# Kernel optimization log

Measured on AMD Instinct MI355X. Metric: run time of the kernel, lower is better.

The kernel has to match this reference:

```python
import jax, jax.numpy as jnp
import numpy as np
from jax import lax

B, C, H, W, HEADS = 2, 256, 192, 256, 8
HS = C // 2  # hidden_size per axial branch


def setup_inputs() -> dict:
    key = jax.random.key(0)
    ks = jax.random.split(key, 12)
    f = lambda k, shape, s=0.02: jax.random.normal(k, shape, jnp.float32) * s
    return {
        "x": jax.random.normal(ks[0], (B, C, H, W), jnp.float32),
        "ln1_g": jnp.ones((C,), jnp.float32),
        "ln1_b": jnp.zeros((C,), jnp.float32),
        "conv_in_w": f(ks[1], (C, C)),
        "conv_in_b": jnp.zeros((C,), jnp.float32),
        "qkv_h_w": f(ks[2], (3 * HS, HS)),
        "qkv_h_b": jnp.zeros((3 * HS,), jnp.float32),
        "qkv_v_w": f(ks[3], (3 * HS, HS)),
        "qkv_v_b": jnp.zeros((3 * HS,), jnp.float32),
        "fuse_w": f(ks[4], (C, C)),
        "fuse_b": jnp.zeros((C,), jnp.float32),
        "ln2_g": jnp.ones((C,), jnp.float32),
        "ln2_b": jnp.zeros((C,), jnp.float32),
        "fc1_w": f(ks[5], (4 * C, C)),
        "fc1_b": f(ks[6], (4 * C,), 1e-6),
        "fc2_w": f(ks[7], (C, 4 * C)),
        "fc2_b": f(ks[8], (C,), 1e-6),
        "peg_w": f(ks[9], (C, 1, 3, 3)),
        "peg_b": jnp.zeros((C,), jnp.float32),
    }


def _ln(x, g, b, eps=1e-5):
    m = x.mean(-1, keepdims=True)
    v = jnp.mean((x - m) ** 2, axis=-1, keepdims=True)
    return (x - m) / jnp.sqrt(v + eps) * g + b


def _mha(q, k, v, heads):
    # q,k,v: [Bn, N, Ch]
    Bn, N, Ch = q.shape
    d = Ch // heads
    q = q.reshape(Bn, N, heads, d).transpose(0, 2, 1, 3)
    k = k.reshape(Bn, N, heads, d).transpose(0, 2, 1, 3)
    v = v.reshape(Bn, N, heads, d).transpose(0, 2, 1, 3)
    scores = jnp.einsum('bhnd,bhmd->bhnm', q, k) / jnp.sqrt(jnp.float32(d))
    probs = jax.nn.softmax(scores, axis=-1)
    out = jnp.einsum('bhnm,bhmd->bhnd', probs, v)
    return out.transpose(0, 2, 1, 3).reshape(Bn, N, Ch)


def reference(x, ln1_g, ln1_b, conv_in_w, conv_in_b, qkv_h_w, qkv_h_b,
              qkv_v_w, qkv_v_b, fuse_w, fuse_b, ln2_g, ln2_b,
              fc1_w, fc1_b, fc2_w, fc2_b, peg_w, peg_b):
    Bx, Cx, Hx, Wx = x.shape
    hs = Cx // 2
    h0 = x
    # LayerNorm over channel dim
    t = x.reshape(Bx, Cx, Hx * Wx).transpose(0, 2, 1)  # [B, HW, C]
    t = _ln(t, ln1_g, ln1_b)
    xn = t.transpose(0, 2, 1).reshape(Bx, Cx, Hx, Wx)
    # 1x1 conv input
    ci = jnp.einsum('bchw,oc->bohw', xn, conv_in_w) + conv_in_b[None, :, None, None]
    # horizontal strips: [B*H, W, hs]; vertical strips: [B*W, H, hs]
    fh = ci[:, :hs].transpose(0, 2, 3, 1).reshape(Bx * Hx, Wx, hs)
    fv = ci[:, hs:].transpose(0, 3, 2, 1).reshape(Bx * Wx, Hx, hs)
    q_h, k_h, v_h = jnp.split(fh @ qkv_h_w.T + qkv_h_b, 3, axis=2)
    q_v, k_v, v_v = jnp.split(fv @ qkv_v_w.T + qkv_v_b, 3, axis=2)
    ah = _mha(q_h, k_h, v_h, HEADS)  # [B*H, W, hs]
    av = _mha(q_v, k_v, v_v, HEADS)  # [B*W, H, hs]
    ah = ah.reshape(Bx, Hx, Wx, hs).transpose(0, 3, 1, 2)  # [B, hs, H, W]
    av = av.reshape(Bx, Wx, Hx, hs).transpose(0, 3, 2, 1)  # [B, hs, H, W]
    cat = jnp.concatenate((ah, av), axis=1)  # [B, C, H, W]
    attn_out = jnp.einsum('bchw,oc->bohw', cat, fuse_w) + fuse_b[None, :, None, None]
    x1 = attn_out + h0
    # FFN
    t = x1.reshape(Bx, Cx, Hx * Wx).transpose(0, 2, 1)  # [B, HW, C]
    h1 = t
    t2 = _ln(t, ln2_g, ln2_b)
    t2 = jax.nn.gelu(t2 @ fc1_w.T + fc1_b, approximate=False)
    t2 = t2 @ fc2_w.T + fc2_b
    t = t2 + h1
    x2 = t.transpose(0, 2, 1).reshape(Bx, Cx, Hx, Wx)
    # PEG: depthwise 3x3 conv + residual
    peg = lax.conv_general_dilated(
        x2, peg_w, window_strides=(1, 1), padding='SAME',
        dimension_numbers=('NCHW', 'OIHW', 'NCHW'), feature_group_count=Cx)
    return peg + peg_b[None, :, None, None] + x2
```

## Files before the change

kernel.cpp:

```cpp
#include <hip/hip_runtime.h>

#define B_ 2
#define C_ 256
#define H_ 192
#define W_ 256
#define HW_ 49152
#define T_ 98304

typedef __bf16 bf16x8 __attribute__((ext_vector_type(8)));
typedef float  f32x4  __attribute__((ext_vector_type(4)));
typedef short  s16x8  __attribute__((ext_vector_type(8)));

__device__ inline unsigned short f2bf(float f) {
    unsigned u = __float_as_uint(f);
    u = u + 0x7fffu + ((u >> 16) & 1u);
    return (unsigned short)(u >> 16);
}
__device__ inline float bf2f(unsigned short u) {
    return __uint_as_float(((unsigned)u) << 16);
}
__device__ inline unsigned short bfbits(float f) {
    __bf16 h = (__bf16)f;
    return __builtin_bit_cast(unsigned short, h);
}

__global__ __launch_bounds__(256) void wcvt_kernel(
    const float* __restrict__ in, unsigned short* __restrict__ out, int n)
{
    int i = (blockIdx.x * 256 + threadIdx.x) * 4;
    if (i >= n) return;
    float4 v = *(const float4*)(in + i);
    out[i + 0] = f2bf(v.x);
    out[i + 1] = f2bf(v.y);
    out[i + 2] = f2bf(v.z);
    out[i + 3] = f2bf(v.w);
}

__global__ __launch_bounds__(256) void ln1_stats_kernel(
    const float* __restrict__ x, float* __restrict__ mean, float* __restrict__ rstd)
{
    int t = blockIdx.x * 256 + threadIdx.x;
    int b = t / HW_;
    int hw = t - b * HW_;
    const float* p = x + (size_t)b * C_ * HW_ + hw;
    float s = 0.f, q = 0.f;
    for (int c = 0; c < C_; ++c) {
        float v = p[(size_t)c * HW_];
        s += v; q += v * v;
    }
    float m = s * (1.f / C_);
    float var = q * (1.f / C_) - m * m;
    mean[t] = m;
    rstd[t] = rsqrtf(var + 1e-5f);
}

__global__ __launch_bounds__(256) void ln2_stats_kernel(
    const float* __restrict__ xr, float* __restrict__ mean, float* __restrict__ rstd)
{
    int wv = threadIdx.x >> 6, lane = threadIdx.x & 63;
    int t = blockIdx.x * 4 + wv;
    const float4 v = *(const float4*)(xr + (size_t)t * C_ + lane * 4);
    float s = v.x + v.y + v.z + v.w;
    float q = v.x * v.x + v.y * v.y + v.z * v.z + v.w * v.w;
    #pragma unroll
    for (int o = 32; o > 0; o >>= 1) {
        s += __shfl_xor(s, o);
        q += __shfl_xor(q, o);
    }
    if (lane == 0) {
        float m = s * (1.f / C_);
        float var = q * (1.f / C_) - m * m;
        mean[t] = m;
        rstd[t] = rsqrtf(var + 1e-5f);
    }
}

__global__ __launch_bounds__(256) void xln_kernel(
    const float* __restrict__ x, const float* __restrict__ mean,
    const float* __restrict__ rstd, const float* __restrict__ g,
    const float* __restrict__ bta, unsigned short* __restrict__ xn)
{
    __shared__ float tile[32][33];
    int t0 = blockIdx.x * 32;
    int c0 = blockIdx.y * 32;
    int b = t0 / HW_, hw0 = t0 - b * HW_;
    int tid = threadIdx.x, lane = tid & 31, grp = tid >> 5;
    float mm = mean[t0 + lane], rr = rstd[t0 + lane];
    #pragma unroll
    for (int j = 0; j < 4; ++j) {
        int c = grp + j * 8;
        float v = x[((size_t)b * C_ + c0 + c) * HW_ + hw0 + lane];
        tile[c][lane] = (v - mm) * rr;
    }
    __syncthreads();
    float gg = g[c0 + lane], bb = bta[c0 + lane];
    #pragma unroll
    for (int j = 0; j < 4; ++j) {
        int tt = grp + j * 8;
        xn[(size_t)(t0 + tt) * C_ + c0 + lane] = f2bf(tile[lane][tt] * gg + bb);
    }
}

enum { AB_ROW = 0, AB_CAT = 1, AB_GATHER = 2, AF32_LN = 3 };
enum { EB_BF16 = 0, EB_F32 = 1, EG_BF16 = 2, ER_F32 = 3 };

template<int AMODE, int EMODE>
__global__ __launch_bounds__(256) void mgemm(
    const unsigned short* __restrict__ A0, const unsigned short* __restrict__ A1,
    const float* __restrict__ Af,
    const unsigned short* __restrict__ Wb, const float* __restrict__ bias,
    const float* __restrict__ mean, const float* __restrict__ rstd,
    const float* __restrict__ lng, const float* __restrict__ lnb,
    const float* __restrict__ resid, float* __restrict__ outf,
    unsigned short* __restrict__ outb,
    int K, int lda, int ldw, int ldo, int rowoff)
{
    __shared__ __align__(16) short As[8][512];
    __shared__ __align__(16) short Bs[8][512];
    const int tid = threadIdx.x;
    const int t0 = blockIdx.x * 128;
    const int n0 = blockIdx.y * 128;
    const int lane = tid & 63, wv = tid >> 6;
    const int wr = wv >> 1, wc = wv & 1;

    f32x4 acc[4][4];
    #pragma unroll
    for (int m = 0; m < 4; ++m)
        #pragma unroll
        for (int n = 0; n < 4; ++n)
            acc[m][n] = (f32x4){0.f, 0.f, 0.f, 0.f};

    for (int k0 = 0; k0 < K; k0 += 32) {
        #pragma unroll
        for (int ic = 0; ic < 2; ++ic) {
            const int c = ic * 256 + tid;
            const int r = c >> 2;
            const int kk = (c & 3) * 8;
            const int slot = (((r & 15) | ((kk >> 3) << 4))) * 8;
            s16x8 v;
            if (AMODE == AF32_LN) {
                const float* src = Af + (size_t)(t0 + r) * lda + k0 + kk;
                float4 v0 = *(const float4*)src;
                float4 v1 = *(const float4*)(src + 4);
                const float mm = mean[t0 + r], rr = rstd[t0 + r];
                float4 g0 = *(const float4*)(lng + k0 + kk);
                float4 g1 = *(const float4*)(lng + k0 + kk + 4);
                float4 b0 = *(const float4*)(lnb + k0 + kk);
                float4 b1 = *(const float4*)(lnb + k0 + kk + 4);
                v[0] = (short)f2bf((v0.x - mm) * rr * g0.x + b0.x);
                v[1] = (short)f2bf((v0.y - mm) * rr * g0.y + b0.y);
                v[2] = (short)f2bf((v0.z - mm) * rr * g0.z + b0.z);
                v[3] = (short)f2bf((v0.w - mm) * rr * g0.w + b0.w);
                v[4] = (short)f2bf((v1.x - mm) * rr * g1.x + b1.x);
                v[5] = (short)f2bf((v1.y - mm) * rr * g1.y + b1.y);
                v[6] = (short)f2bf((v1.z - mm) * rr * g1.z + b1.z);
                v[7] = (short)f2bf((v1.w - mm) * rr * g1.w + b1.w);
            } else {
                const unsigned short* src;
                if (AMODE == AB_CAT) {
                    src = (k0 < 128)
                        ? A0 + (size_t)(t0 + r) * 128 + k0 + kk
                        : A1 + (size_t)(t0 + r) * 128 + (k0 - 128) + kk;
                } else if (AMODE == AB_GATHER) {
                    const int gr = rowoff + t0 + r;
                    const int b = gr / HW_;
                    const int rem = gr - b * HW_;
                    const int w = rem / H_;
                    const int h = rem - w * H_;
                    src = A0 + ((size_t)b * HW_ + (size_t)h * W_ + w) * 256
                          + 128 + k0 + kk;
                } else {
                    src = A0 + (size_t)(t0 + r) * lda + k0 + kk;
                }
                v = *(const s16x8*)src;
            }
            *(s16x8*)&As[r >> 4][slot] = v;
            s16x8 wv8 = *(const s16x8*)(Wb + (size_t)(n0 + r) * ldw + k0 + kk);
            *(s16x8*)&Bs[r >> 4][slot] = wv8;
        }
        __syncthreads();
        bf16x8 af[4], bfr[4];
        #pragma unroll
        for (int m = 0; m < 4; ++m)
            af[m] = __builtin_bit_cast(bf16x8, *(const s16x8*)&As[wr * 4 + m][lane * 8]);
        #pragma unroll
        for (int n = 0; n < 4; ++n)
            bfr[n] = __builtin_bit_cast(bf16x8, *(const s16x8*)&Bs[wc * 4 + n][lane * 8]);
        #pragma unroll
        for (int m = 0; m < 4; ++m)
            #pragma unroll
            for (int n = 0; n < 4; ++n)
                acc[m][n] = __builtin_amdgcn_mfma_f32_16x16x32_bf16(
                    af[m], bfr[n], acc[m][n], 0, 0, 0);
        __syncthreads();
    }

    const int rowb = t0 + wr * 64 + (lane >> 4) * 4;
    const int colb = n0 + wc * 64 + (lane & 15);
    #pragma unroll
    for (int n = 0; n < 4; ++n) {
        const int col = colb + n * 16;
        const float bcol = bias[col];
        #pragma unroll
        for (int m = 0; m < 4; ++m) {
            #pragma unroll
            for (int r = 0; r < 4; ++r) {
                const int row = rowb + m * 16 + r;
                float v = acc[m][n][r] + bcol;
                if (EMODE == EG_BF16)
                    v = 0.5f * v * (1.f + erff(v * 0.70710678118654752f));
                if (EMODE == ER_F32)
                    v += resid[(size_t)row * 256 + col];
                if (EMODE == EB_F32 || EMODE == ER_F32)
                    outf[(size_t)row * ldo + col] = v;
                else
                    outb[(size_t)row * ldo + col] = f2bf(v);
            }
        }
    }
}

__global__ __launch_bounds__(256) void tadd_kernel(
    const float* __restrict__ x, float* __restrict__ x1)
{
    __shared__ float tile[32][33];
    int t0 = blockIdx.x * 32;
    int c0 = blockIdx.y * 32;
    int b = t0 / HW_, hw0 = t0 - b * HW_;
    int tid = threadIdx.x;
    int lane = tid & 31, grp = tid >> 5;
    #pragma unroll
    for (int j = 0; j < 4; ++j) {
        int c = grp + j * 8;
        tile[c][lane] = x[((size_t)b * C_ + c0 + c) * HW_ + hw0 + lane];
    }
    __syncthreads();
    #pragma unroll
    for (int j = 0; j < 4; ++j) {
        int tt = grp + j * 8;
        x1[(size_t)(t0 + tt) * C_ + c0 + lane] += tile[lane][tt];
    }
}

template<int N, int DIR>
__global__ __launch_bounds__(256) void attn_mfma_kernel(
    const unsigned short* __restrict__ qkv, unsigned short* __restrict__ outb, int strip0)
{
    constexpr int NT = N / 16;
    constexpr int CH = N / 32;
    constexpr int QTW = N / 64;
    constexpr int PST = N + 8;
    __shared__ __align__(16) short kls[NT * 256];
    __shared__ __align__(16) short vls[CH * 512];
    __shared__ __align__(16) short plds[4 * 16 * PST];
    const int head = blockIdx.x & 7;
    const int sl = blockIdx.x >> 3;
    const int s = strip0 + sl;
    const int tid = threadIdx.x;
    const unsigned short* base = qkv + (size_t)sl * N * 384;
    for (int i = tid; i < 2 * N; i += 256) {
        int r = i >> 1, hf = i & 1;
        s16x8 kv = *(const s16x8*)(base + (size_t)r * 384 + 128 + head * 16 + hf * 8);
        *(s16x8*)&kls[(r >> 4) * 256 + (hf * 16 + (r & 15)) * 8] = kv;
    }
    for (int i = tid; i < 2 * N; i += 256) {
        int r = i >> 1, hf = i & 1;
        s16x8 vv = *(const s16x8*)(base + (size_t)r * 384 + 256 + head * 16 + hf * 8);
        short* dst = &vls[(r >> 5) * 512 + ((r & 31) >> 3) * 128 + (r & 7)];
        #pragma unroll
        for (int j = 0; j < 8; ++j)
            dst[(hf * 8 + j) * 8] = vv[j];
    }
    __syncthreads();
    const int wv = tid >> 6, lane = tid & 63, g = lane >> 4, q = lane & 15;
    short* myP = &plds[wv * 16 * PST];
    const bf16x8 zf = __builtin_bit_cast(bf16x8, (s16x8){0,0,0,0,0,0,0,0});
    for (int qt_i = 0; qt_i < QTW; ++qt_i) {
        const int q0 = wv * (N / 4) + qt_i * 16;
        bf16x8 qf = zf;
        if (lane < 32)
            qf = __builtin_bit_cast(bf16x8,
                *(const s16x8*)(base + (size_t)(q0 + q) * 384 + head * 16 + g * 8));
        f32x4 sc[NT];
        #pragma unroll
        for (int n = 0; n < NT; ++n) {
            bf16x8 kf = zf;
            if (lane < 32)
                kf = __builtin_bit_cast(bf16x8, *(const s16x8*)&kls[n * 256 + lane * 8]);
            sc[n] = __builtin_amdgcn_mfma_f32_16x16x32_bf16(
                kf, qf, (f32x4){0.f, 0.f, 0.f, 0.f}, 0, 0, 0);
        }
        float mx = -3.0e38f;
        #pragma unroll
        for (int n = 0; n < NT; ++n)
            mx = fmaxf(mx, fmaxf(fmaxf(sc[n][0], sc[n][1]), fmaxf(sc[n][2], sc[n][3])));
        mx = fmaxf(mx, __shfl_xor(mx, 16));
        mx = fmaxf(mx, __shfl_xor(mx, 32));
        float sum = 0.f;
        #pragma unroll
        for (int n = 0; n < NT; ++n) {
            float p0 = __expf((sc[n][0] - mx) * 0.25f);
            float p1 = __expf((sc[n][1] - mx) * 0.25f);
            float p2 = __expf((sc[n][2] - mx) * 0.25f);
            float p3 = __expf((sc[n][3] - mx) * 0.25f);
            sum += (p0 + p1) + (p2 + p3);
            unsigned u01 = ((unsigned)bfbits(p1) << 16) | bfbits(p0);
            unsigned u23 = ((unsigned)bfbits(p3) << 16) | bfbits(p2);
            *(unsigned*)&myP[q * PST + n * 16 + g * 4] = u01;
            *(unsigned*)&myP[q * PST + n * 16 + g * 4 + 2] = u23;
        }
        sum += __shfl_xor(sum, 16);
        sum += __shfl_xor(sum, 32);
        const float inv = 1.f / sum;
        f32x4 o = (f32x4){0.f, 0.f, 0.f, 0.f};
        #pragma unroll
        for (int c = 0; c < CH; ++c) {
            bf16x8 vf = __builtin_bit_cast(bf16x8, *(const s16x8*)&vls[c * 512 + lane * 8]);
            bf16x8 pf = __builtin_bit_cast(bf16x8, *(const s16x8*)&myP[q * PST + c * 32 + g * 8]);
            o = __builtin_amdgcn_mfma_f32_16x16x32_bf16(vf, pf, o, 0, 0, 0);
        }
        unsigned lo = ((unsigned)bfbits(o[1] * inv) << 16) | bfbits(o[0] * inv);
        unsigned hi = ((unsigned)bfbits(o[3] * inv) << 16) | bfbits(o[2] * inv);
        size_t dst;
        if (DIR == 0) {
            dst = ((size_t)s * W_ + q0 + q) * 128 + head * 16 + g * 4;
        } else {
            int b = s >> 8, w = s & 255;
            dst = ((size_t)b * HW_ + (size_t)(q0 + q) * W_ + w) * 128 + head * 16 + g * 4;
        }
        *(uint2*)&outb[dst] = make_uint2(lo, hi);
    }
}

__global__ __launch_bounds__(256) void peg_kernel(
    const float* __restrict__ x2t, const float* __restrict__ pw,
    const float* __restrict__ pb, float* __restrict__ outp)
{
    __shared__ float pwt[9][132];
    __shared__ float tile[128][36];
    const int t0 = blockIdx.x * 32;
    const int cbase = blockIdx.y * 128;
    const int b = t0 / HW_, hw0 = t0 - b * HW_;
    const int h = hw0 >> 8, w0 = hw0 & 255;
    const int tid = threadIdx.x;
    for (int i = tid; i < 1152; i += 256) {
        int tap = i >> 7, ch = i & 127;
        pwt[tap][ch] = pw[(size_t)(cbase + ch) * 9 + tap];
    }
    __syncthreads();
    const int c4 = tid & 31;
    const int tg = tid >> 5;
    const int cq = cbase + c4 * 4;
    float4 pb4 = *(const float4*)(pb + cq);
    #pragma unroll
    for (int j = 0; j < 4; ++j) {
        int tt = tg * 4 + j;
        int t = t0 + tt;
        int w = w0 + tt;
        float4 a = *(const float4*)(x2t + (size_t)t * C_ + cq);
        a.x += pb4.x; a.y += pb4.y; a.z += pb4.z; a.w += pb4.w;
        #pragma unroll
        for (int dh = -1; dh <= 1; ++dh) {
            int hh = h + dh;
            if (hh < 0 || hh >= H_) continue;
            #pragma unroll
            for (int dw = -1; dw <= 1; ++dw) {
                int ww = w + dw;
                if (ww < 0 || ww >= W_) continue;
                float4 xv = *(const float4*)(x2t + (size_t)(t + dh * W_ + dw) * C_ + cq);
                float4 wv = *(const float4*)&pwt[(dh + 1) * 3 + (dw + 1)][c4 * 4];
                a.x += wv.x * xv.x; a.y += wv.y * xv.y;
                a.z += wv.z * xv.z; a.w += wv.w * xv.w;
            }
        }
        tile[c4 * 4 + 0][tt] = a.x;
        tile[c4 * 4 + 1][tt] = a.y;
        tile[c4 * 4 + 2][tt] = a.z;
        tile[c4 * 4 + 3][tt] = a.w;
    }
    __syncthreads();
    const int ch = tid >> 1, hf = (tid & 1) * 16;
    float* drow = outp + ((size_t)b * C_ + cbase + ch) * HW_ + hw0 + hf;
    #pragma unroll
    for (int qq = 0; qq < 4; ++qq) {
        float4 vv = make_float4(tile[ch][hf + qq * 4 + 0], tile[ch][hf + qq * 4 + 1],
                                tile[ch][hf + qq * 4 + 2], tile[ch][hf + qq * 4 + 3]);
        *(float4*)(drow + qq * 4) = vv;
    }
}

extern "C" void kernel_launch(void* const* d_in, const int* in_sizes, int n_in,
                              void* d_out, int out_size, void* d_ws, size_t ws_size,
                              hipStream_t stream)
{
    (void)in_sizes; (void)n_in; (void)out_size; (void)ws_size;
    const float* x         = (const float*)d_in[0];
    const float* ln1_g     = (const float*)d_in[1];
    const float* ln1_b     = (const float*)d_in[2];
    const float* conv_in_w = (const float*)d_in[3];
    const float* conv_in_b = (const float*)d_in[4];
    const float* qkv_h_w   = (const float*)d_in[5];
    const float* qkv_h_b   = (const float*)d_in[6];
    const float* qkv_v_w   = (const float*)d_in[7];
    const float* qkv_v_b   = (const float*)d_in[8];
    const float* fuse_w    = (const float*)d_in[9];
    const float* fuse_b    = (const float*)d_in[10];
    const float* ln2_g     = (const float*)d_in[11];
    const float* ln2_b     = (const float*)d_in[12];
    const float* fc1_w     = (const float*)d_in[13];
    const float* fc1_b     = (const float*)d_in[14];
    const float* fc2_w     = (const float*)d_in[15];
    const float* fc2_b     = (const float*)d_in[16];
    const float* peg_w     = (const float*)d_in[17];
    const float* peg_b     = (const float*)d_in[18];
    float* outp = (float*)d_out;

    float* wsf   = (float*)d_ws;
    float* mean1 = wsf;
    float* rstd1 = wsf + (size_t)T_;
    float* mean2 = wsf + 2 * (size_t)T_;
    float* rstd2 = wsf + 3 * (size_t)T_;
    float* x1    = wsf + 4 * (size_t)T_;
    unsigned short* xn = (unsigned short*)x1;
    unsigned short* ci = (unsigned short*)(x1 + (size_t)T_ * 128);
    unsigned short* ah = (unsigned short*)(x1 + (size_t)T_ * 256);
    unsigned short* av = ah + (size_t)T_ * 128;
    unsigned short* qt = av + (size_t)T_ * 128;
    unsigned short* wb = qt + (size_t)12288 * 1024;
    unsigned short* wconv = wb;
    unsigned short* wqh   = wconv + 65536;
    unsigned short* wqv   = wqh + 49152;
    unsigned short* wfu   = wqv + 49152;
    unsigned short* wf1   = wfu + 65536;
    unsigned short* wf2   = wf1 + 262144;

    dim3 blk(256);

    wcvt_kernel<<<dim3(64), blk, 0, stream>>>(conv_in_w, wconv, 65536);
    wcvt_kernel<<<dim3(48), blk, 0, stream>>>(qkv_h_w, wqh, 49152);
    wcvt_kernel<<<dim3(48), blk, 0, stream>>>(qkv_v_w, wqv, 49152);
    wcvt_kernel<<<dim3(64), blk, 0, stream>>>(fuse_w, wfu, 65536);
    wcvt_kernel<<<dim3(256), blk, 0, stream>>>(fc1_w, wf1, 262144);
    wcvt_kernel<<<dim3(256), blk, 0, stream>>>(fc2_w, wf2, 262144);
    ln1_stats_kernel<<<dim3(T_ / 256), blk, 0, stream>>>(x, mean1, rstd1);
    xln_kernel<<<dim3(T_ / 32, 8), blk, 0, stream>>>(x, mean1, rstd1, ln1_g, ln1_b, xn);
    mgemm<AB_ROW, EB_BF16><<<dim3(768, 2), blk, 0, stream>>>(
        xn, nullptr, nullptr, wconv, conv_in_b, nullptr, nullptr, nullptr, nullptr,
        nullptr, nullptr, ci, 256, 256, 256, 256, 0);
    for (int ch = 0; ch < 4; ++ch) {
        const size_t r0 = (size_t)ch * 24576;
        mgemm<AB_ROW, EB_BF16><<<dim3(192, 3), blk, 0, stream>>>(
            ci + r0 * 256, nullptr, nullptr, wqh, qkv_h_b, nullptr, nullptr, nullptr,
            nullptr, nullptr, nullptr, qt, 128, 256, 128, 384, 0);
        attn_mfma_kernel<256, 0><<<dim3(96 * 8), blk, 0, stream>>>(qt, ah, ch * 96);
    }
    for (int cv = 0; cv < 4; ++cv) {
        mgemm<AB_GATHER, EB_BF16><<<dim3(192, 3), blk, 0, stream>>>(
            ci, nullptr, nullptr, wqv, qkv_v_b, nullptr, nullptr, nullptr,
            nullptr, nullptr, nullptr, qt, 128, 0, 128, 384, cv * 24576);
        attn_mfma_kernel<192, 1><<<dim3(128 * 8), blk, 0, stream>>>(qt, av, cv * 128);
    }
    mgemm<AB_CAT, EB_F32><<<dim3(768, 2), blk, 0, stream>>>(
        ah, av, nullptr, wfu, fuse_b, nullptr, nullptr, nullptr, nullptr,
        nullptr, x1, nullptr, 256, 128, 256, 256, 0);
    tadd_kernel<<<dim3(T_ / 32, 8), blk, 0, stream>>>(x, x1);
    ln2_stats_kernel<<<dim3(T_ / 4), blk, 0, stream>>>(x1, mean2, rstd2);
    for (int cs = 0; cs < 8; ++cs) {
        const size_t r0 = (size_t)cs * 12288;
        mgemm<AF32_LN, EG_BF16><<<dim3(96, 8), blk, 0, stream>>>(
            nullptr, nullptr, x1 + r0 * 256, wf1, fc1_b, mean2 + r0, rstd2 + r0,
            ln2_g, ln2_b, nullptr, nullptr, qt, 256, 256, 256, 1024, 0);
        mgemm<AB_ROW, ER_F32><<<dim3(96, 2), blk, 0, stream>>>(
            qt, nullptr, nullptr, wf2, fc2_b, nullptr, nullptr, nullptr, nullptr,
            x1 + r0 * 256, x1 + r0 * 256, nullptr, 1024, 1024, 1024, 256, 0);
    }
    peg_kernel<<<dim3(T_ / 32, 2), blk, 0, stream>>>(x1, peg_w, peg_b, outp);
}
```

Baseline: 1.198 ms.

## Use direct global-to-LDS loads in GEMM, precompute LN2 output, enlarge chunks

Replaces the register-staged A/B tile loads in the GEMM with buffer loads that write straight to LDS (global_load_lds, 16 bytes per lane), with row pointers and the gather addresses computed once per block. LayerNorm2 is split out into its own kernel that writes normalized bf16 rows, so the fc1 GEMM no longer applies the norm per tile. The attention and FFN loops use larger chunks, which means fewer launches and a larger qt scratch buffer. The PEG kernel's shared tile is transposed so results are stored as float4. This adds an extra bf16 write and read for LN2 and relies on the LDS-load layout matching the existing fragment slot pattern.

```diff
diff --git a/kernel.cpp b/kernel.cpp
--- a/kernel.cpp
+++ b/kernel.cpp
@@ -22,6 +22,11 @@
 __device__ inline unsigned short bfbits(float f) {
     __bf16 h = (__bf16)f;
     return __builtin_bit_cast(unsigned short, h);
+}
+__device__ inline void gload_lds16(const unsigned short* g, short* l) {
+    __builtin_amdgcn_global_load_lds(
+        (const __attribute__((address_space(1))) unsigned int*)g,
+        (__attribute__((address_space(3))) unsigned int*)l, 16, 0, 0);
 }
 
 __global__ __launch_bounds__(256) void wcvt_kernel(
@@ -54,27 +59,6 @@
     rstd[t] = rsqrtf(var + 1e-5f);
 }
 
-__global__ __launch_bounds__(256) void ln2_stats_kernel(
-    const float* __restrict__ xr, float* __restrict__ mean, float* __restrict__ rstd)
-{
-    int wv = threadIdx.x >> 6, lane = threadIdx.x & 63;
-    int t = blockIdx.x * 4 + wv;
-    const float4 v = *(const float4*)(xr + (size_t)t * C_ + lane * 4);
-    float s = v.x + v.y + v.z + v.w;
-    float q = v.x * v.x + v.y * v.y + v.z * v.z + v.w * v.w;
-    #pragma unroll
-    for (int o = 32; o > 0; o >>= 1) {
-        s += __shfl_xor(s, o);
-        q += __shfl_xor(q, o);
-    }
-    if (lane == 0) {
-        float m = s * (1.f / C_);
-        float var = q * (1.f / C_) - m * m;
-        mean[t] = m;
-        rstd[t] = rsqrtf(var + 1e-5f);
-    }
-}
-
 __global__ __launch_bounds__(256) void xln_kernel(
     const float* __restrict__ x, const float* __restrict__ mean,
     const float* __restrict__ rstd, const float* __restrict__ g,
@@ -101,16 +85,40 @@
     }
 }
 
-enum { AB_ROW = 0, AB_CAT = 1, AB_GATHER = 2, AF32_LN = 3 };
+__global__ __launch_bounds__(256) void ln2norm_kernel(
+    const float* __restrict__ xr, const float* __restrict__ g,
+    const float* __restrict__ bta, unsigned short* __restrict__ out)
+{
+    int wv = threadIdx.x >> 6, lane = threadIdx.x & 63;
+    int t = blockIdx.x * 4 + wv;
+    const float4 v = *(const float4*)(xr + (size_t)t * C_ + lane * 4);
+    float s = v.x + v.y + v.z + v.w;
+    float q = v.x * v.x + v.y * v.y + v.z * v.z + v.w * v.w;
+    #pragma unroll
+    for (int o = 32; o > 0; o >>= 1) {
+        s += __shfl_xor(s, o);
+        q += __shfl_xor(q, o);
+    }
+    float m = s * (1.f / C_);
+    float r = rsqrtf(q * (1.f / C_) - m * m + 1e-5f);
+    float4 gg = *(const float4*)(g + lane * 4);
+    float4 bb = *(const float4*)(bta + lane * 4);
+    unsigned short o0 = f2bf((v.x - m) * r * gg.x + bb.x);
+    unsigned short o1 = f2bf((v.y - m) * r * gg.y + bb.y);
+    unsigned short o2 = f2bf((v.z - m) * r * gg.z + bb.z);
+    unsigned short o3 = f2bf((v.w - m) * r * gg.w + bb.w);
+    unsigned lo = ((unsigned)o1 << 16) | o0;
+    unsigned hi = ((unsigned)o3 << 16) | o2;
+    *(uint2*)(out + (size_t)t * C_ + lane * 4) = make_uint2(lo, hi);
+}
+
+enum { AB_ROW = 0, AB_CAT = 1, AB_GATHER = 2 };
 enum { EB_BF16 = 0, EB_F32 = 1, EG_BF16 = 2, ER_F32 = 3 };
 
 template<int AMODE, int EMODE>
 __global__ __launch_bounds__(256) void mgemm(
     const unsigned short* __restrict__ A0, const unsigned short* __restrict__ A1,
-    const float* __restrict__ Af,
     const unsigned short* __restrict__ Wb, const float* __restrict__ bias,
-    const float* __restrict__ mean, const float* __restrict__ rstd,
-    const float* __restrict__ lng, const float* __restrict__ lnb,
     const float* __restrict__ resid, float* __restrict__ outf,
     unsigned short* __restrict__ outb,
     int K, int lda, int ldw, int ldo, int rowoff)
@@ -122,6 +130,29 @@
     const int n0 = blockIdx.y * 128;
     const int lane = tid & 63, wv = tid >> 6;
     const int wr = wv >> 1, wc = wv & 1;
+    const int fr = lane & 15;
+    const int fk = (lane >> 4) * 8;
+
+    const unsigned short* aptr0 = nullptr;
+    const unsigned short* aptr1 = nullptr;
+    if (AMODE == AB_GATHER) {
+        #pragma unroll
+        for (int si = 0; si < 2; ++si) {
+            const int gr = rowoff + t0 + (wv * 2 + si) * 16 + fr;
+            const int b = gr / HW_;
+            const int rem = gr - b * HW_;
+            const int w = rem / H_;
+            const int h = rem - w * H_;
+            const unsigned short* p =
+                A0 + ((size_t)b * HW_ + (size_t)h * W_ + w) * 256 + 128 + fk;
+            if (si == 0) aptr0 = p; else aptr1 = p;
+        }
+    } else if (AMODE == AB_ROW) {
+        aptr0 = A0 + (size_t)(t0 + (wv * 2 + 0) * 16 + fr) * lda + fk;
+        aptr1 = A0 + (size_t)(t0 + (wv * 2 + 1) * 16 + fr) * lda + fk;
+    }
+    const unsigned short* bptr0 = Wb + (size_t)(n0 + (wv * 2 + 0) * 16 + fr) * ldw + fk;
+    const unsigned short* bptr1 = Wb + (size_t)(n0 + (wv * 2 + 1) * 16 + fr) * ldw + fk;
 
     f32x4 acc[4][4];
     #pragma unroll
@@ -131,53 +162,19 @@
             acc[m][n] = (f32x4){0.f, 0.f, 0.f, 0.f};
 
     for (int k0 = 0; k0 < K; k0 += 32) {
-        #pragma unroll
-        for (int ic = 0; ic < 2; ++ic) {
-            const int c = ic * 256 + tid;
-            const int r = c >> 2;
-            const int kk = (c & 3) * 8;
-            const int slot = (((r & 15) | ((kk >> 3) << 4))) * 8;
-            s16x8 v;
-            if (AMODE == AF32_LN) {
-                const float* src = Af + (size_t)(t0 + r) * lda + k0 + kk;
-                float4 v0 = *(const float4*)src;
-                float4 v1 = *(const float4*)(src + 4);
-                const float mm = mean[t0 + r], rr = rstd[t0 + r];
-                float4 g0 = *(const float4*)(lng + k0 + kk);
-                float4 g1 = *(const float4*)(lng + k0 + kk + 4);
-                float4 b0 = *(const float4*)(lnb + k0 + kk);
-                float4 b1 = *(const float4*)(lnb + k0 + kk + 4);
-                v[0] = (short)f2bf((v0.x - mm) * rr * g0.x + b0.x);
-                v[1] = (short)f2bf((v0.y - mm) * rr * g0.y + b0.y);
-                v[2] = (short)f2bf((v0.z - mm) * rr * g0.z + b0.z);
-                v[3] = (short)f2bf((v0.w - mm) * rr * g0.w + b0.w);
-                v[4] = (short)f2bf((v1.x - mm) * rr * g1.x + b1.x);
-                v[5] = (short)f2bf((v1.y - mm) * rr * g1.y + b1.y);
-                v[6] = (short)f2bf((v1.z - mm) * rr * g1.z + b1.z);
-                v[7] = (short)f2bf((v1.w - mm) * rr * g1.w + b1.w);
-            } else {
-                const unsigned short* src;
-                if (AMODE == AB_CAT) {
-                    src = (k0 < 128)
-                        ? A0 + (size_t)(t0 + r) * 128 + k0 + kk
-                        : A1 + (size_t)(t0 + r) * 128 + (k0 - 128) + kk;
-                } else if (AMODE == AB_GATHER) {
-                    const int gr = rowoff + t0 + r;
-                    const int b = gr / HW_;
-                    const int rem = gr - b * HW_;
-                    const int w = rem / H_;
-                    const int h = rem - w * H_;
-                    src = A0 + ((size_t)b * HW_ + (size_t)h * W_ + w) * 256
-                          + 128 + k0 + kk;
-                } else {
-                    src = A0 + (size_t)(t0 + r) * lda + k0 + kk;
-                }
-                v = *(const s16x8*)src;
-            }
-            *(s16x8*)&As[r >> 4][slot] = v;
-            s16x8 wv8 = *(const s16x8*)(Wb + (size_t)(n0 + r) * ldw + k0 + kk);
-            *(s16x8*)&Bs[r >> 4][slot] = wv8;
-        }
+        if (AMODE == AB_CAT) {
+            const unsigned short* base = (k0 < 128) ? A0 : A1;
+            const int kk = (k0 & 127) + fk;
+            gload_lds16(base + (size_t)(t0 + (wv * 2 + 0) * 16 + fr) * 128 + kk,
+                        &As[wv * 2 + 0][0]);
+            gload_lds16(base + (size_t)(t0 + (wv * 2 + 1) * 16 + fr) * 128 + kk,
+                        &As[wv * 2 + 1][0]);
+        } else {
+            gload_lds16(aptr0 + k0, &As[wv * 2 + 0][0]);
+            gload_lds16(aptr1 + k0, &As[wv * 2 + 1][0]);
+        }
+        gload_lds16(bptr0 + k0, &Bs[wv * 2 + 0][0]);
+        gload_lds16(bptr1 + k0, &Bs[wv * 2 + 1][0]);
         __syncthreads();
         bf16x8 af[4], bfr[4];
         #pragma unroll
@@ -337,7 +334,7 @@
     const float* __restrict__ pb, float* __restrict__ outp)
 {
     __shared__ float pwt[9][132];
-    __shared__ float tile[128][36];
+    __shared__ float tile[32][132];
     const int t0 = blockIdx.x * 32;
     const int cbase = blockIdx.y * 128;
     const int b = t0 / HW_, hw0 = t0 - b * HW_;
@@ -368,23 +365,20 @@
                 int ww = w + dw;
                 if (ww < 0 || ww >= W_) continue;
                 float4 xv = *(const float4*)(x2t + (size_t)(t + dh * W_ + dw) * C_ + cq);
-                float4 wv = *(const float4*)&pwt[(dh + 1) * 3 + (dw + 1)][c4 * 4];
-                a.x += wv.x * xv.x; a.y += wv.y * xv.y;
-                a.z += wv.z * xv.z; a.w += wv.w * xv.w;
+                float4 wvv = *(const float4*)&pwt[(dh + 1) * 3 + (dw + 1)][c4 * 4];
+                a.x += wvv.x * xv.x; a.y += wvv.y * xv.y;
+                a.z += wvv.z * xv.z; a.w += wvv.w * xv.w;
             }
         }
-        tile[c4 * 4 + 0][tt] = a.x;
-        tile[c4 * 4 + 1][tt] = a.y;
-        tile[c4 * 4 + 2][tt] = a.z;
-        tile[c4 * 4 + 3][tt] = a.w;
+        *(float4*)&tile[tt][c4 * 4] = a;
     }
     __syncthreads();
     const int ch = tid >> 1, hf = (tid & 1) * 16;
     float* drow = outp + ((size_t)b * C_ + cbase + ch) * HW_ + hw0 + hf;
     #pragma unroll
     for (int qq = 0; qq < 4; ++qq) {
-        float4 vv = make_float4(tile[ch][hf + qq * 4 + 0], tile[ch][hf + qq * 4 + 1],
-                                tile[ch][hf + qq * 4 + 2], tile[ch][hf + qq * 4 + 3]);
+        float4 vv = make_float4(tile[hf + qq * 4 + 0][ch], tile[hf + qq * 4 + 1][ch],
+                                tile[hf + qq * 4 + 2][ch], tile[hf + qq * 4 + 3][ch]);
         *(float4*)(drow + qq * 4) = vv;
     }
 }
@@ -418,15 +412,14 @@
     float* wsf   = (float*)d_ws;
     float* mean1 = wsf;
     float* rstd1 = wsf + (size_t)T_;
-    float* mean2 = wsf + 2 * (size_t)T_;
-    float* rstd2 = wsf + 3 * (size_t)T_;
-    float* x1    = wsf + 4 * (size_t)T_;
+    float* x1    = wsf + 2 * (size_t)T_;
     unsigned short* xn = (unsigned short*)x1;
     unsigned short* ci = (unsigned short*)(x1 + (size_t)T_ * 128);
     unsigned short* ah = (unsigned short*)(x1 + (size_t)T_ * 256);
     unsigned short* av = ah + (size_t)T_ * 128;
+    unsigned short* xn2 = ah;
     unsigned short* qt = av + (size_t)T_ * 128;
-    unsigned short* wb = qt + (size_t)12288 * 1024;
+    unsigned short* wb = qt + (size_t)24576 * 1024;
     unsigned short* wconv = wb;
     unsigned short* wqh   = wconv + 65536;
     unsigned short* wqv   = wqh + 49152;
@@ -445,34 +438,32 @@
     ln1_stats_kernel<<<dim3(T_ / 256), blk, 0, stream>>>(x, mean1, rstd1);
     xln_kernel<<<dim3(T_ / 32, 8), blk, 0, stream>>>(x, mean1, rstd1, ln1_g, ln1_b, xn);
     mgemm<AB_ROW, EB_BF16><<<dim3(768, 2), blk, 0, stream>>>(
-        xn, nullptr, nullptr, wconv, conv_in_b, nullptr, nullptr, nullptr, nullptr,
-        nullptr, nullptr, ci, 256, 256, 256, 256, 0);
-    for (int ch = 0; ch < 4; ++ch) {
-        const size_t r0 = (size_t)ch * 24576;
-        mgemm<AB_ROW, EB_BF16><<<dim3(192, 3), blk, 0, stream>>>(
-            ci + r0 * 256, nullptr, nullptr, wqh, qkv_h_b, nullptr, nullptr, nullptr,
-            nullptr, nullptr, nullptr, qt, 128, 256, 128, 384, 0);
-        attn_mfma_kernel<256, 0><<<dim3(96 * 8), blk, 0, stream>>>(qt, ah, ch * 96);
-    }
-    for (int cv = 0; cv < 4; ++cv) {
-        mgemm<AB_GATHER, EB_BF16><<<dim3(192, 3), blk, 0, stream>>>(
-            ci, nullptr, nullptr, wqv, qkv_v_b, nullptr, nullptr, nullptr,
-            nullptr, nullptr, nullptr, qt, 128, 0, 128, 384, cv * 24576);
-        attn_mfma_kernel<192, 1><<<dim3(128 * 8), blk, 0, stream>>>(qt, av, cv * 128);
+        xn, nullptr, wconv, conv_in_b, nullptr, nullptr, ci, 256, 256, 256, 256, 0);
+    for (int ch = 0; ch < 2; ++ch) {
+        const size_t r0 = (size_t)ch * 49152;
+        mgemm<AB_ROW, EB_BF16><<<dim3(384, 3), blk, 0, stream>>>(
+            ci + r0 * 256, nullptr, wqh, qkv_h_b, nullptr, nullptr, qt,
+            128, 256, 128, 384, 0);
+        attn_mfma_kernel<256, 0><<<dim3(192 * 8), blk, 0, stream>>>(qt, ah, ch * 192);
+    }
+    for (int cv = 0; cv < 2; ++cv) {
+        mgemm<AB_GATHER, EB_BF16><<<dim3(384, 3), blk, 0, stream>>>(
+            ci, nullptr, wqv, qkv_v_b, nullptr, nullptr, qt,
+            128, 0, 128, 384, cv * 49152);
+        attn_mfma_kernel<192, 1><<<dim3(256 * 8), blk, 0, stream>>>(qt, av, cv * 256);
     }
     mgemm<AB_CAT, EB_F32><<<dim3(768, 2), blk, 0, stream>>>(
-        ah, av, nullptr, wfu, fuse_b, nullptr, nullptr, nullptr, nullptr,
-        nullptr, x1, nullptr, 256, 128, 256, 256, 0);
+        ah, av, wfu, fuse_b, nullptr, x1, nullptr, 256, 128, 256, 256, 0);
     tadd_kernel<<<dim3(T_ / 32, 8), blk, 0, stream>>>(x, x1);
-    ln2_stats_kernel<<<dim3(T_ / 4), blk, 0, stream>>>(x1, mean2, rstd2);
-    for (int cs = 0; cs < 8; ++cs) {
-        const size_t r0 = (size_t)cs * 12288;
-        mgemm<AF32_LN, EG_BF16><<<dim3(96, 8), blk, 0, stream>>>(
-            nullptr, nullptr, x1 + r0 * 256, wf1, fc1_b, mean2 + r0, rstd2 + r0,
-            ln2_g, ln2_b, nullptr, nullptr, qt, 256, 256, 256, 1024, 0);
-        mgemm<AB_ROW, ER_F32><<<dim3(96, 2), blk, 0, stream>>>(
-            qt, nullptr, nullptr, wf2, fc2_b, nullptr, nullptr, nullptr, nullptr,
-            x1 + r0 * 256, x1 + r0 * 256, nullptr, 1024, 1024, 1024, 256, 0);
+    ln2norm_kernel<<<dim3(T_ / 4), blk, 0, stream>>>(x1, ln2_g, ln2_b, xn2);
+    for (int cs = 0; cs < 4; ++cs) {
+        const size_t r0 = (size_t)cs * 24576;
+        mgemm<AB_ROW, EG_BF16><<<dim3(192, 8), blk, 0, stream>>>(
+            xn2 + r0 * 256, nullptr, wf1, fc1_b, nullptr, nullptr, qt,
+            256, 256, 256, 1024, 0);
+        mgemm<AB_ROW, ER_F32><<<dim3(192, 2), blk, 0, stream>>>(
+            qt, nullptr, wf2, fc2_b, x1 + r0 * 256, x1 + r0 * 256, nullptr,
+            1024, 1024, 1024, 256, 0);
     }
     peg_kernel<<<dim3(T_ / 32, 2), blk, 0, stream>>>(x1, peg_w, peg_b, outp);
 }
```

Result: faster. 1.075 ms (-10.3%).
